# Optimization experiments

Measured on AMD Instinct MI355X. Metric: run time of the kernel, lower is better.

Reference implementation:

```python
import jax, jax.numpy as jnp
import numpy as np

D_MODEL = 768
H = 12
D_FF = 3072
EPS = 1e-6


def _layernorm(x, alpha, bias):
    # torch.std default is Bessel-corrected (ddof=1); denom is (std + eps)
    mean = jnp.mean(x, axis=-1, keepdims=True)
    var = jnp.sum((x - mean) ** 2, axis=-1, keepdims=True) / (x.shape[-1] - 1)
    std = jnp.sqrt(var)
    return alpha * (x - mean) / (std + EPS) + bias


def _linear(x, w, b):
    # torch nn.Linear: y = x @ W.T + b, W is [out, in]
    return jnp.einsum('...i,oi->...o', x, w) + b


def setup_inputs() -> dict:
    key = jax.random.key(0)
    ks = jax.random.split(key, 16)
    B, S = 8, 1024
    sc = 1.0 / np.sqrt(D_MODEL)
    inp = {
        'x': jax.random.normal(ks[0], (B, S, D_MODEL), dtype=jnp.float32),
        'mask': jax.random.randint(ks[1], (B, 1, 1, S), 0, 2, dtype=jnp.int32),
        'wq': jax.random.normal(ks[2], (D_MODEL, D_MODEL), dtype=jnp.float32) * sc,
        'bq': jnp.zeros((D_MODEL,), jnp.float32),
        'wk': jax.random.normal(ks[3], (D_MODEL, D_MODEL), dtype=jnp.float32) * sc,
        'bk': jnp.zeros((D_MODEL,), jnp.float32),
        'wv': jax.random.normal(ks[4], (D_MODEL, D_MODEL), dtype=jnp.float32) * sc,
        'bv': jnp.zeros((D_MODEL,), jnp.float32),
        'wo': jax.random.normal(ks[5], (D_MODEL, D_MODEL), dtype=jnp.float32) * sc,
        'bo': jnp.zeros((D_MODEL,), jnp.float32),
        'ln1_a': jnp.ones((D_MODEL,), jnp.float32),
        'ln1_b': jnp.zeros((D_MODEL,), jnp.float32),
        'ln2_a': jnp.ones((D_MODEL,), jnp.float32),
        'ln2_b': jnp.zeros((D_MODEL,), jnp.float32),
        'w1': jax.random.normal(ks[6], (D_FF, D_MODEL), dtype=jnp.float32) * sc,
        'b1': jnp.zeros((D_FF,), jnp.float32),
        'w2': jax.random.normal(ks[7], (D_MODEL, D_FF), dtype=jnp.float32) * (1.0 / np.sqrt(D_FF)),
        'b2': jnp.zeros((D_MODEL,), jnp.float32),
    }
    return inp


def reference(x, mask, wq, bq, wk, bk, wv, bv, wo, bo,
              ln1_a, ln1_b, ln2_a, ln2_b, w1, b1, w2, b2):
    B, S, _ = x.shape
    d_k = D_MODEL // H

    # --- residual 1: pre-LN self-attention (dropout identity at eval) ---
    xn = _layernorm(x, ln1_a, ln1_b)
    q = _linear(xn, wq, bq).reshape(B, S, H, d_k).transpose(0, 2, 1, 3)
    k = _linear(xn, wk, bk).reshape(B, S, H, d_k).transpose(0, 2, 1, 3)
    v = _linear(xn, wv, bv).reshape(B, S, H, d_k).transpose(0, 2, 1, 3)

    scores = jnp.einsum('bhqd,bhkd->bhqk', q, k) / jnp.sqrt(jnp.float32(d_k))
    # faithful quirk: masked positions set to 1e-9, NOT -inf
    scores = jnp.where(mask == 0, jnp.float32(1e-9), scores)
    attn = jax.nn.softmax(scores, axis=-1)
    ctx = jnp.einsum('bhqk,bhkd->bhqd', attn, v)
    ctx = ctx.transpose(0, 2, 1, 3).reshape(B, S, D_MODEL)
    x = x + _linear(ctx, wo, bo)

    # --- residual 2: pre-LN feed-forward ---
    xn = _layernorm(x, ln2_a, ln2_b)
    ff = _linear(jax.nn.relu(_linear(xn, w1, b1)), w2, b2)
    return x + ff
```

## Files before the change

kernel.cpp:

```cpp
#include <hip/hip_runtime.h>
#include <stdint.h>

#define D_MODEL 768
#define D_FF    3072
#define NH      12
#define DK      64
#define BB      8
#define SS      1024
#define NTOK    (BB*SS)
#define QST     2304

typedef float          f32x4  __attribute__((ext_vector_type(4)));
typedef __bf16         bf16x8 __attribute__((ext_vector_type(8)));
typedef unsigned short us8v   __attribute__((ext_vector_type(8)));
typedef unsigned short us4v   __attribute__((ext_vector_type(4)));

__device__ __forceinline__ unsigned short f2b(float f) {
  unsigned int u = __builtin_bit_cast(unsigned int, f);
  u = (u + 0x7fffu + ((u >> 16) & 1u)) >> 16;
  return (unsigned short)u;
}
__device__ __forceinline__ float b2f(unsigned short h) {
  unsigned int u = ((unsigned int)h) << 16;
  return __builtin_bit_cast(float, u);
}
__device__ __forceinline__ float exp2a(float x) {
  float r; asm("v_exp_f32 %0, %1" : "=v"(r) : "v"(x)); return r;
}
__device__ __forceinline__ unsigned int cvtpk(float lo, float hi) {
  unsigned int r;
  asm("v_cvt_pk_bf16_f32 %0, %1, %2" : "=v"(r) : "v"(lo), "v"(hi));
  return r;
}
__device__ __forceinline__ void waitv3() {
  asm volatile("s_waitcnt vmcnt(3)" ::: "memory");
}
__device__ __forceinline__ void waitv0() {
  asm volatile("s_waitcnt vmcnt(0)" ::: "memory");
}

#define N4TOT 1769472
__global__ __launch_bounds__(256) void cast6_kernel(
    const float* __restrict__ s0, const float* __restrict__ s1,
    const float* __restrict__ s2, const float* __restrict__ s3,
    const float* __restrict__ s4, const float* __restrict__ s5,
    unsigned short* __restrict__ d0, unsigned short* __restrict__ d1,
    unsigned short* __restrict__ d2, unsigned short* __restrict__ d3,
    unsigned short* __restrict__ d4, unsigned short* __restrict__ d5) {
  int i = blockIdx.x * 256 + threadIdx.x;
  if (i >= N4TOT) return;
  const float* src; unsigned short* dst; int off;
  if (i < 147456)       { src = s0; dst = d0; off = i; }
  else if (i < 294912)  { src = s1; dst = d1; off = i - 147456; }
  else if (i < 442368)  { src = s2; dst = d2; off = i - 294912; }
  else if (i < 589824)  { src = s3; dst = d3; off = i - 442368; }
  else if (i < 1179648) { src = s4; dst = d4; off = i - 589824; }
  else                  { src = s5; dst = d5; off = i - 1179648; }
  float4 f = ((const float4*)src)[off];
  us4v o; o.x = f2b(f.x); o.y = f2b(f.y); o.z = f2b(f.z); o.w = f2b(f.w);
  *(us4v*)(dst + (size_t)off * 4) = o;
}

__global__ __launch_bounds__(256) void ln_kernel(const float* __restrict__ x,
                                                 const float* __restrict__ ga,
                                                 const float* __restrict__ gb,
                                                 unsigned short* __restrict__ y) {
  int row = blockIdx.x;
  const float* xr = x + (size_t)row * D_MODEL;
  int t = threadIdx.x, w = t >> 6, l = t & 63;
  float v0 = xr[t], v1 = xr[t + 256], v2 = xr[t + 512];
  float s = v0 + v1 + v2;
  #pragma unroll
  for (int off = 32; off; off >>= 1) s += __shfl_xor(s, off);
  __shared__ float red[4];
  __shared__ float stats[2];
  if (l == 0) red[w] = s;
  __syncthreads();
  if (t == 0) stats[0] = (red[0] + red[1] + red[2] + red[3]) * (1.0f / 768.0f);
  __syncthreads();
  float mean = stats[0];
  float d0 = v0 - mean, d1 = v1 - mean, d2 = v2 - mean;
  float ss = d0 * d0 + d1 * d1 + d2 * d2;
  #pragma unroll
  for (int off = 32; off; off >>= 1) ss += __shfl_xor(ss, off);
  __syncthreads();
  if (l == 0) red[w] = ss;
  __syncthreads();
  if (t == 0) {
    float tot = red[0] + red[1] + red[2] + red[3];
    stats[1] = 1.0f / (sqrtf(tot * (1.0f / 767.0f)) + 1e-6f);
  }
  __syncthreads();
  float inv = stats[1];
  unsigned short* yr = y + (size_t)row * D_MODEL;
  yr[t]       = f2b(ga[t]       * (d0 * inv) + gb[t]);
  yr[t + 256] = f2b(ga[t + 256] * (d1 * inv) + gb[t + 256]);
  yr[t + 512] = f2b(ga[t + 512] * (d2 * inv) + gb[t + 512]);
}

#define GLDS(g, l) __builtin_amdgcn_global_load_lds( \
    (__attribute__((address_space(1))) const void*)(g), \
    (__attribute__((address_space(3))) void*)(l), 16, 0, 0)

template<int BN>
__global__ __launch_bounds__(256) void gemm_t(
    const unsigned short* __restrict__ A,
    const unsigned short* __restrict__ W,
    const float* __restrict__ biasA,
    const float* __restrict__ biasB,
    const float* __restrict__ biasC,
    int segw,
    const float* __restrict__ resid,
    float* __restrict__ outF,
    unsigned short* __restrict__ outB,
    int M, int N, int K, int relu) {
  constexpr int WC = (BN == 128) ? 2 : 1;
  constexpr int MF = (BN == 128) ? 4 : 2;
  constexpr int NF = 4;
  constexpr int NBUF = (BN == 128) ? 2 : 3;
  constexpr int ASZ = 128 * 32;
  constexpr int BSZ = BN * 32;
  __shared__ unsigned short As[NBUF * ASZ];
  __shared__ unsigned short Bs[NBUF * BSZ];
  int t = threadIdx.x;
  int w = t >> 6, l = t & 63;
  int brow = blockIdx.x * 128;
  int bcol = blockIdx.y * BN;
  int wr = (w / WC) * (MF * 16);
  int wc = (w % WC) * (NF * 16);

  const unsigned short* ga0 = A + (size_t)(brow + (t >> 2)) * K + (t & 3) * 8;
  const unsigned short* ga1 = ga0 + (size_t)64 * K;
  const unsigned short* gb0 = W + (size_t)(bcol + (t >> 2)) * K + (t & 3) * 8;
  const unsigned short* gb1 = gb0 + (size_t)64 * K;

  f32x4 acc[MF][NF];
  #pragma unroll
  for (int m = 0; m < MF; m++)
    #pragma unroll
    for (int n = 0; n < NF; n++)
      acc[m][n] = (f32x4){0.f, 0.f, 0.f, 0.f};

  int arow = wr + (l & 15);
  int bcw  = wc + (l & 15);
  int kk   = (l >> 4) * 8;
  const int nt = K / 32;

  auto stage = [&](int ti, int buf) {
    int k0 = ti * 32;
    GLDS(ga0 + k0, As + buf * ASZ + t * 8);
    GLDS(ga1 + k0, As + buf * ASZ + 2048 + t * 8);
    GLDS(gb0 + k0, Bs + buf * BSZ + t * 8);
    if constexpr (BN == 128) GLDS(gb1 + k0, Bs + buf * BSZ + 2048 + t * 8);
  };

  if constexpr (NBUF == 3) {
    stage(0, 0);
    stage(1, 1);
    waitv3();
    __builtin_amdgcn_s_barrier();
    __builtin_amdgcn_sched_barrier(0);
  } else {
    stage(0, 0);
    __syncthreads();
  }

  int cb = 0, sb = 2;
  for (int ti = 0; ti < nt; ti++) {
    if constexpr (NBUF == 3) {
      if (ti + 2 < nt) { stage(ti + 2, sb); sb = (sb == 2) ? 0 : sb + 1; }
    } else {
      if (ti + 1 < nt) stage(ti + 1, cb ^ 1);
    }
    bf16x8 af[MF], bfv[NF];
    #pragma unroll
    for (int m = 0; m < MF; m++)
      af[m] = *(const bf16x8*)(As + cb * ASZ + (arow + m * 16) * 32 + kk);
    #pragma unroll
    for (int n = 0; n < NF; n++)
      bfv[n] = *(const bf16x8*)(Bs + cb * BSZ + (bcw + n * 16) * 32 + kk);
    #pragma unroll
    for (int m = 0; m < MF; m++)
      #pragma unroll
      for (int n = 0; n < NF; n++)
        acc[m][n] = __builtin_amdgcn_mfma_f32_16x16x32_bf16(af[m], bfv[n], acc[m][n], 0, 0, 0);
    if constexpr (NBUF == 3) {
      if (ti + 2 < nt)      waitv3();
      else if (ti + 1 < nt) waitv0();
      if (ti + 1 < nt) {
        __builtin_amdgcn_s_barrier();
        __builtin_amdgcn_sched_barrier(0);
      }
      cb = (cb == 2) ? 0 : cb + 1;
    } else {
      if (ti + 1 < nt) __syncthreads();
      cb ^= 1;
    }
  }

  #pragma unroll
  for (int n = 0; n < NF; n++) {
    int col = bcol + wc + n * 16 + (l & 15);
    int seg = col / segw, off = col - seg * segw;
    const float* bp = (seg == 0) ? biasA : ((seg == 1) ? biasB : biasC);
    float bv = bp[off];
    #pragma unroll
    for (int m = 0; m < MF; m++) {
      int row0 = brow + wr + m * 16 + (l >> 4) * 4;
      #pragma unroll
      for (int r = 0; r < 4; r++) {
        int row = row0 + r;
        float vacc = acc[m][n][r] + bv;
        if (resid) vacc += resid[(size_t)row * N + col];
        if (relu)  vacc = fmaxf(vacc, 0.f);
        if (outF)  outF[(size_t)row * N + col] = vacc;
        if (outB)  outB[(size_t)row * N + col] = f2b(vacc);
      }
    }
  }
}

#define PPAD 72
#define KPAD 72
#define SM_C1 0.18033688011112043f
#define SM_C2 1.4426950408889634e-9f

__global__ __launch_bounds__(256) void attn_mfma(
    const unsigned short* __restrict__ qkv,
    const int* __restrict__ mask,
    unsigned short* __restrict__ ctx) {
  int bh = blockIdx.x;
  int qt = blockIdx.y;
  int b = bh / NH, h = bh % NH;
  int t = threadIdx.x, w = t >> 6, l = t & 63;
  int ql = l & 15, g = l >> 4;

  const unsigned short* kp = qkv + 768 + h * DK;
  const unsigned short* vp = qkv + 1536 + h * DK;

  __shared__ unsigned short Ks[4096];
  __shared__ unsigned short Vt[64 * KPAD];
  __shared__ unsigned short Ps[128 * PPAD];
  __shared__ float mk01[64];
  __shared__ float corrw[4][2][16];
  __shared__ float lrw[4][2][16];

  int srow = t >> 3;
  int sblk = t & 7;
  int sb0  = sblk ^ (srow & 7);
  int sb1  = sblk ^ ((srow + 32) & 7);

  bf16x8 qf[2][2];
  {
    const unsigned short* qp = qkv + h * DK;
    size_t row0 = (size_t)(b * SS + qt * 128 + w * 32 + ql);
    #pragma unroll
    for (int s = 0; s < 2; s++)
      #pragma unroll
      for (int ks = 0; ks < 2; ks++)
        qf[s][ks] = *(const bf16x8*)(qp + (row0 + s * 16) * QST + ks * 32 + g * 8);
  }

  f32x4 acc_o[2][4];
  #pragma unroll
  for (int s = 0; s < 2; s++)
    #pragma unroll
    for (int nf = 0; nf < 4; nf++) acc_o[s][nf] = (f32x4){0.f, 0.f, 0.f, 0.f};
  float mrun[2] = {-INFINITY, -INFINITY};
  float lrun[2] = {0.f, 0.f};

  for (int kt = 0; kt < 16; kt++) {
    size_t tok0 = (size_t)(b * SS + kt * 64);
    GLDS(kp + (tok0 + srow)      * QST + sb0 * 8, Ks + t * 8);
    GLDS(kp + (tok0 + srow + 32) * QST + sb1 * 8, Ks + 2048 + t * 8);
    {
      const unsigned short* vsrc = vp + (tok0 + l) * QST + w * 16;
      us8v v0 = *(const us8v*)vsrc;
      us8v v1 = *(const us8v*)(vsrc + 8);
      #pragma unroll
      for (int j = 0; j < 8; j++) {
        Vt[(w * 16 + j)     * KPAD + l] = v0[j];
        Vt[(w * 16 + 8 + j) * KPAD + l] = v1[j];
      }
    }
    if (t < 64) mk01[t] = mask[b * SS + kt * 64 + t] ? 1.0f : 0.0f;
    __syncthreads();

    f32x4 sa[2][4];
    #pragma unroll
    for (int s = 0; s < 2; s++)
      #pragma unroll
      for (int kf = 0; kf < 4; kf++) sa[s][kf] = (f32x4){0.f, 0.f, 0.f, 0.f};
    #pragma unroll
    for (int ks = 0; ks < 2; ks++) {
      bf16x8 kfr[4];
      #pragma unroll
      for (int kf = 0; kf < 4; kf++) {
        int row = kf * 16 + ql;
        kfr[kf] = *(const bf16x8*)(Ks + row * 64 + ((g + 4 * ks) ^ (ql & 7)) * 8);
      }
      #pragma unroll
      for (int s = 0; s < 2; s++)
        #pragma unroll
        for (int kf = 0; kf < 4; kf++)
          sa[s][kf] = __builtin_amdgcn_mfma_f32_16x16x32_bf16(kfr[kf], qf[s][ks], sa[s][kf], 0, 0, 0);
    }

    #pragma unroll
    for (int s = 0; s < 2; s++) {
      float pv[16];
      float tm = -INFINITY;
      #pragma unroll
      for (int kf = 0; kf < 4; kf++)
        #pragma unroll
        for (int r = 0; r < 4; r++) {
          float m01 = mk01[kf * 16 + g * 4 + r];
          float xm = sa[s][kf][r] * SM_C1 - SM_C2;
          float sc = fmaf(m01, xm, SM_C2);
          pv[kf * 4 + r] = sc;
          tm = fmaxf(tm, sc);
        }
      tm = fmaxf(tm, __shfl_xor(tm, 16));
      tm = fmaxf(tm, __shfl_xor(tm, 32));
      float mn = fmaxf(mrun[s], tm);
      float corr = exp2a(mrun[s] - mn);
      float rs = 0.f;
      #pragma unroll
      for (int i = 0; i < 16; i++) { pv[i] = exp2a(pv[i] - mn); rs += pv[i]; }
      rs += __shfl_xor(rs, 16);
      rs += __shfl_xor(rs, 32);
      mrun[s] = mn;
      lrun[s] = lrun[s] * corr + rs;

      int prow = w * 32 + s * 16 + ql;
      #pragma unroll
      for (int kf = 0; kf < 4; kf++) {
        uint2 pk;
        pk.x = cvtpk(pv[kf * 4 + 0], pv[kf * 4 + 1]);
        pk.y = cvtpk(pv[kf * 4 + 2], pv[kf * 4 + 3]);
        *(uint2*)(Ps + prow * PPAD + kf * 16 + g * 4) = pk;
      }
      if (l < 16) corrw[w][s][l] = corr;
    }

    #pragma unroll
    for (int s = 0; s < 2; s++) {
      float cb0 = corrw[w][s][g * 4 + 0], cb1 = corrw[w][s][g * 4 + 1];
      float cb2 = corrw[w][s][g * 4 + 2], cb3 = corrw[w][s][g * 4 + 3];
      #pragma unroll
      for (int nf = 0; nf < 4; nf++) {
        acc_o[s][nf][0] *= cb0; acc_o[s][nf][1] *= cb1;
        acc_o[s][nf][2] *= cb2; acc_o[s][nf][3] *= cb3;
      }
    }
    #pragma unroll
    for (int ks = 0; ks < 2; ks++) {
      bf16x8 vfr[4];
      #pragma unroll
      for (int nf = 0; nf < 4; nf++)
        vfr[nf] = *(const bf16x8*)(Vt + (ql + nf * 16) * KPAD + g * 8 + ks * 32);
      #pragma unroll
      for (int s = 0; s < 2; s++) {
        bf16x8 pa = *(const bf16x8*)(Ps + (w * 32 + s * 16 + ql) * PPAD + g * 8 + ks * 32);
        #pragma unroll
        for (int nf = 0; nf < 4; nf++)
          acc_o[s][nf] = __builtin_amdgcn_mfma_f32_16x16x32_bf16(pa, vfr[nf], acc_o[s][nf], 0, 0, 0);
      }
    }
    __syncthreads();
  }

  #pragma unroll
  for (int s = 0; s < 2; s++)
    if (l < 16) lrw[w][s][l] = lrun[s];
  #pragma unroll
  for (int s = 0; s < 2; s++) {
    float li0 = 1.0f / lrw[w][s][g * 4 + 0], li1 = 1.0f / lrw[w][s][g * 4 + 1];
    float li2 = 1.0f / lrw[w][s][g * 4 + 2], li3 = 1.0f / lrw[w][s][g * 4 + 3];
    #pragma unroll
    for (int nf = 0; nf < 4; nf++) {
      #pragma unroll
      for (int r = 0; r < 4; r++) {
        float li = (r == 0) ? li0 : (r == 1) ? li1 : (r == 2) ? li2 : li3;
        int tok = b * SS + qt * 128 + w * 32 + s * 16 + g * 4 + r;
        ctx[(size_t)tok * D_MODEL + h * DK + nf * 16 + ql] = f2b(acc_o[s][nf][r] * li);
      }
    }
  }
}

extern "C" void kernel_launch(void* const* d_in, const int* in_sizes, int n_in,
                              void* d_out, int out_size, void* d_ws, size_t ws_size,
                              hipStream_t stream) {
  const float* x    = (const float*)d_in[0];
  const int*   mask = (const int*)d_in[1];
  const float* wq   = (const float*)d_in[2];
  const float* bq   = (const float*)d_in[3];
  const float* wk   = (const float*)d_in[4];
  const float* bk   = (const float*)d_in[5];
  const float* wv   = (const float*)d_in[6];
  const float* bv   = (const float*)d_in[7];
  const float* wo   = (const float*)d_in[8];
  const float* bo   = (const float*)d_in[9];
  const float* ln1a = (const float*)d_in[10];
  const float* ln1b = (const float*)d_in[11];
  const float* ln2a = (const float*)d_in[12];
  const float* ln2b = (const float*)d_in[13];
  const float* w1   = (const float*)d_in[14];
  const float* b1   = (const float*)d_in[15];
  const float* w2   = (const float*)d_in[16];
  const float* b2   = (const float*)d_in[17];

  char* ws = (char*)d_ws;
  unsigned short* wqkvb = (unsigned short*)(ws + 0);
  unsigned short* wob   = (unsigned short*)(ws + 3538944);
  unsigned short* w1b   = (unsigned short*)(ws + 4718592);
  unsigned short* w2b   = (unsigned short*)(ws + 9437184);
  unsigned short* xnb   = (unsigned short*)(ws + 14155776);
  unsigned short* qkvb  = (unsigned short*)(ws + 26738688);
  unsigned short* ctxb  = (unsigned short*)(ws + 64487424);
  float*          x1    = (float*)(ws + 26738688);
  unsigned short* h1b   = (unsigned short*)(ws + 51904512);

  cast6_kernel<<<N4TOT / 256, 256, 0, stream>>>(
      wq, wk, wv, wo, w1, w2,
      wqkvb, wqkvb + 589824, wqkvb + 1179648, wob, w1b, w2b);

  ln_kernel<<<NTOK, 256, 0, stream>>>(x, ln1a, ln1b, xnb);

  dim3 gqkv(NTOK / 128, QST / 128);
  gemm_t<128><<<gqkv, 256, 0, stream>>>(xnb, wqkvb, bq, bk, bv, 768,
                                        nullptr, nullptr, qkvb,
                                        NTOK, QST, D_MODEL, 0);

  dim3 ga(BB * NH, SS / 128);
  attn_mfma<<<ga, 256, 0, stream>>>(qkvb, mask, ctxb);

  dim3 gwo(NTOK / 128, D_MODEL / 64);
  gemm_t<64><<<gwo, 256, 0, stream>>>(ctxb, wob, bo, nullptr, nullptr, D_MODEL,
                                      x, x1, nullptr,
                                      NTOK, D_MODEL, D_MODEL, 0);

  ln_kernel<<<NTOK, 256, 0, stream>>>(x1, ln2a, ln2b, xnb);

  dim3 gff(NTOK / 128, D_FF / 128);
  gemm_t<128><<<gff, 256, 0, stream>>>(xnb, w1b, b1, nullptr, nullptr, D_FF,
                                       nullptr, nullptr, h1b,
                                       NTOK, D_FF, D_MODEL, 1);

  dim3 gff2(NTOK / 128, D_MODEL / 64);
  gemm_t<64><<<gff2, 256, 0, stream>>>(h1b, w2b, b2, nullptr, nullptr, D_MODEL,
                                       x1, (float*)d_out, nullptr,
                                       NTOK, D_MODEL, D_FF, 0);
}
```

Measured before the change: 297.3 us.

## Use BK=64 with XOR-swizzled LDS and double buffering for BN=64 GEMM

For the BN=64 GEMM variant, the triple-buffered BK=32 pipeline with manual vmcnt waits is replaced by double buffering with a K tile of 64. The LDS layout is XOR-swizzled per row to avoid bank conflicts on the wider rows. This halves the number of barriers per K sweep and does more MFMA work per sync. The cost is one less stage of prefetch depth, so global latency may be less hidden.

Result: faster. 278.9 us (-6.2%).

```diff
diff --git a/kernel.cpp b/kernel.cpp
--- a/kernel.cpp
+++ b/kernel.cpp
@@ -31,12 +31,6 @@
   unsigned int r;
   asm("v_cvt_pk_bf16_f32 %0, %1, %2" : "=v"(r) : "v"(lo), "v"(hi));
   return r;
-}
-__device__ __forceinline__ void waitv3() {
-  asm volatile("s_waitcnt vmcnt(3)" ::: "memory");
-}
-__device__ __forceinline__ void waitv0() {
-  asm volatile("s_waitcnt vmcnt(0)" ::: "memory");
 }
 
 #define N4TOT 1769472
@@ -114,14 +108,14 @@
     float* __restrict__ outF,
     unsigned short* __restrict__ outB,
     int M, int N, int K, int relu) {
-  constexpr int WC = (BN == 128) ? 2 : 1;
-  constexpr int MF = (BN == 128) ? 4 : 2;
-  constexpr int NF = 4;
-  constexpr int NBUF = (BN == 128) ? 2 : 3;
-  constexpr int ASZ = 128 * 32;
-  constexpr int BSZ = BN * 32;
-  __shared__ unsigned short As[NBUF * ASZ];
-  __shared__ unsigned short Bs[NBUF * BSZ];
+  constexpr int BK  = (BN == 128) ? 32 : 64;
+  constexpr int WC  = (BN == 128) ? 2 : 1;
+  constexpr int MF  = (BN == 128) ? 4 : 2;
+  constexpr int NF  = 4;
+  constexpr int ASZ = 128 * BK;
+  constexpr int BSZ = BN * BK;
+  __shared__ unsigned short As[2 * ASZ];
+  __shared__ unsigned short Bs[2 * BSZ];
   int t = threadIdx.x;
   int w = t >> 6, l = t & 63;
   int brow = blockIdx.x * 128;
@@ -129,10 +123,19 @@
   int wr = (w / WC) * (MF * 16);
   int wc = (w % WC) * (NF * 16);
 
-  const unsigned short* ga0 = A + (size_t)(brow + (t >> 2)) * K + (t & 3) * 8;
-  const unsigned short* ga1 = ga0 + (size_t)64 * K;
-  const unsigned short* gb0 = W + (size_t)(bcol + (t >> 2)) * K + (t & 3) * 8;
-  const unsigned short* gb1 = gb0 + (size_t)64 * K;
+  const unsigned short *ga0, *ga1, *gb0, *gb1;
+  if constexpr (BN == 128) {
+    ga0 = A + (size_t)(brow + (t >> 2)) * K + (t & 3) * 8;
+    ga1 = ga0 + (size_t)64 * K;
+    gb0 = W + (size_t)(bcol + (t >> 2)) * K + (t & 3) * 8;
+    gb1 = gb0 + (size_t)64 * K;
+  } else {
+    int r5 = t >> 3;
+    int swz = (t & 7) ^ (r5 & 7);
+    ga0 = A + (size_t)(brow + r5) * K + swz * 8;
+    gb0 = W + (size_t)(bcol + r5) * K + swz * 8;
+    ga1 = gb1 = nullptr;
+  }
 
   f32x4 acc[MF][NF];
   #pragma unroll
@@ -143,59 +146,62 @@
 
   int arow = wr + (l & 15);
   int bcw  = wc + (l & 15);
-  int kk   = (l >> 4) * 8;
-  const int nt = K / 32;
+  int g    = l >> 4;
+  int kk   = g * 8;
+  const int nt = K / BK;
 
   auto stage = [&](int ti, int buf) {
-    int k0 = ti * 32;
-    GLDS(ga0 + k0, As + buf * ASZ + t * 8);
-    GLDS(ga1 + k0, As + buf * ASZ + 2048 + t * 8);
-    GLDS(gb0 + k0, Bs + buf * BSZ + t * 8);
-    if constexpr (BN == 128) GLDS(gb1 + k0, Bs + buf * BSZ + 2048 + t * 8);
+    int k0 = ti * BK;
+    if constexpr (BN == 128) {
+      GLDS(ga0 + k0, As + buf * ASZ + t * 8);
+      GLDS(ga1 + k0, As + buf * ASZ + 2048 + t * 8);
+      GLDS(gb0 + k0, Bs + buf * BSZ + t * 8);
+      GLDS(gb1 + k0, Bs + buf * BSZ + 2048 + t * 8);
+    } else {
+      #pragma unroll
+      for (int i = 0; i < 4; i++)
+        GLDS(ga0 + k0 + (size_t)(32 * i) * K, As + buf * ASZ + i * 2048 + t * 8);
+      #pragma unroll
+      for (int i = 0; i < 2; i++)
+        GLDS(gb0 + k0 + (size_t)(32 * i) * K, Bs + buf * BSZ + i * 2048 + t * 8);
+    }
   };
 
-  if constexpr (NBUF == 3) {
-    stage(0, 0);
-    stage(1, 1);
-    waitv3();
-    __builtin_amdgcn_s_barrier();
-    __builtin_amdgcn_sched_barrier(0);
-  } else {
-    stage(0, 0);
-    __syncthreads();
-  }
-
-  int cb = 0, sb = 2;
+  stage(0, 0);
+  __syncthreads();
+
+  int cb = 0;
   for (int ti = 0; ti < nt; ti++) {
-    if constexpr (NBUF == 3) {
-      if (ti + 2 < nt) { stage(ti + 2, sb); sb = (sb == 2) ? 0 : sb + 1; }
-    } else {
-      if (ti + 1 < nt) stage(ti + 1, cb ^ 1);
-    }
-    bf16x8 af[MF], bfv[NF];
-    #pragma unroll
-    for (int m = 0; m < MF; m++)
-      af[m] = *(const bf16x8*)(As + cb * ASZ + (arow + m * 16) * 32 + kk);
-    #pragma unroll
-    for (int n = 0; n < NF; n++)
-      bfv[n] = *(const bf16x8*)(Bs + cb * BSZ + (bcw + n * 16) * 32 + kk);
-    #pragma unroll
-    for (int m = 0; m < MF; m++)
-      #pragma unroll
-      for (int n = 0; n < NF; n++)
-        acc[m][n] = __builtin_amdgcn_mfma_f32_16x16x32_bf16(af[m], bfv[n], acc[m][n], 0, 0, 0);
-    if constexpr (NBUF == 3) {
-      if (ti + 2 < nt)      waitv3();
-      else if (ti + 1 < nt) waitv0();
-      if (ti + 1 < nt) {
-        __builtin_amdgcn_s_barrier();
-        __builtin_amdgcn_sched_barrier(0);
-      }
-      cb = (cb == 2) ? 0 : cb + 1;
-    } else {
-      if (ti + 1 < nt) __syncthreads();
-      cb ^= 1;
-    }
+    if (ti + 1 < nt) stage(ti + 1, cb ^ 1);
+    #pragma unroll
+    for (int h = 0; h < BK / 32; h++) {
+      bf16x8 af[MF], bfv[NF];
+      #pragma unroll
+      for (int m = 0; m < MF; m++) {
+        int aro = arow + m * 16;
+        if constexpr (BN == 128)
+          af[m] = *(const bf16x8*)(As + cb * ASZ + aro * 32 + kk);
+        else
+          af[m] = *(const bf16x8*)(As + cb * ASZ + aro * 64 +
+                                   ((((h << 2) + g) ^ (l & 7)) << 3));
+      }
+      #pragma unroll
+      for (int n = 0; n < NF; n++) {
+        int bco = bcw + n * 16;
+        if constexpr (BN == 128)
+          bfv[n] = *(const bf16x8*)(Bs + cb * BSZ + bco * 32 + kk);
+        else
+          bfv[n] = *(const bf16x8*)(Bs + cb * BSZ + bco * 64 +
+                                    ((((h << 2) + g) ^ (l & 7)) << 3));
+      }
+      #pragma unroll
+      for (int m = 0; m < MF; m++)
+        #pragma unroll
+        for (int n = 0; n < NF; n++)
+          acc[m][n] = __builtin_amdgcn_mfma_f32_16x16x32_bf16(af[m], bfv[n], acc[m][n], 0, 0, 0);
+    }
+    if (ti + 1 < nt) __syncthreads();
+    cb ^= 1;
   }
 
   #pragma unroll
```
